# Kernel optimization log

Hardware: AMD Instinct MI355X
Metric: run time of the kernel (lower is better)

The kernel has to match this reference:

```python
import jax, jax.numpy as jnp
import numpy as np

PI = np.pi
NDIMS, K, M, F = 3, 513, 65536, 16
H = (K - 1) // 2  # 256; augmented factor has K = 2*H + 1 rows


def setup_inputs() -> dict:
    key = jax.random.key(0)
    k1, k2, k3, k4 = jax.random.split(key, 4)
    x = jax.random.uniform(k1, (M, NDIMS), dtype=jnp.float32)          # samples in [0,1]
    factors_real = jax.random.uniform(k2, (NDIMS, H, F), dtype=jnp.float32)
    factors_imag = 0.1 * jax.random.uniform(k3, (NDIMS, H, F), dtype=jnp.float32)
    lam = jnp.full((F,), 1.0 / F, dtype=jnp.float32)                   # f_vec init in torch
    return {"x": x, "factors_real": factors_real, "factors_imag": factors_imag, "lam": lam}


def _augment(fr, fi):
    # aug_fac real = [R; ones; flip(R)], imag = [I; zeros; -flip(I)]  -> (NDIMS, K, F)
    ones = jnp.ones((NDIMS, 1, F), fr.dtype)
    zeros = jnp.zeros((NDIMS, 1, F), fi.dtype)
    Ar = jnp.concatenate([fr, ones, jnp.flip(fr, axis=1)], axis=1)
    Ai = jnp.concatenate([fi, zeros, -jnp.flip(fi, axis=1)], axis=1)
    return Ar, Ai


def _conditionals(Ar, Ai):
    # c[n, f] = 1 / trapz(relu(Re(bb1^T aug_fac_n))[:, f], t),  t = linspace(0.01, 1, 100)
    T = 100
    t = jnp.linspace(0.01, 1.0, T, dtype=jnp.float32)
    kv = jnp.arange(-H, H + 1, dtype=jnp.float32)
    phi = (2.0 * PI) * kv[:, None] * t[None, :]                         # (K, T)
    # bb1 = exp(-i*phi): Re(bb1^T (Ar + i Ai)) = cos(phi)^T Ar + sin(phi)^T Ai
    y = (jnp.einsum('kt,nkf->ntf', jnp.cos(phi), Ar)
         + jnp.einsum('kt,nkf->ntf', jnp.sin(phi), Ai))
    y = jnp.maximum(y, 0.0)
    dt = jnp.float32((1.0 - 0.01) / (T - 1))
    integral = 0.5 * jnp.sum(y[:, 1:, :] + y[:, :-1, :], axis=1) * dt   # (NDIMS, F)
    return 1.0 / integral


def reference(x, factors_real, factors_imag, lam):
    Ar, Ai = _augment(factors_real, factors_imag)
    # torch computes c from detached data (numpy trapz) -> constant w.r.t. grads
    c = jax.lax.stop_gradient(_conditionals(Ar, Ai))                    # (NDIMS, F)
    kv = jnp.arange(-H, H + 1, dtype=jnp.float32)
    # basis = exp(-i*2pi*k*x): Re(basis^T A) = cos^T Ar + sin^T Ai
    theta = (2.0 * PI) * kv[None, :, None] * jnp.swapaxes(x, 0, 1)[:, None, :]  # (NDIMS, K, M)
    proj = (jnp.einsum('nkm,nkf->nmf', jnp.cos(theta), Ar)
            + jnp.einsum('nkm,nkf->nmf', jnp.sin(theta), Ai))           # (NDIMS, M, F)
    proj = jnp.maximum(proj, 0.0) * c[:, None, :]
    res = jnp.prod(proj, axis=0)                                        # (M, F)
    # sum(res @ diagflat(lam), dim=1) == res @ lam
    return res @ lam
```

## Files before the change

### kernel.cpp

```cpp
#include <hip/hip_runtime.h>

#define NDIMS 3
#define H_HALF 256
#define F_DIM 16
#define PI_F 3.14159265358979323846f

typedef _Float16 half8_t __attribute__((ext_vector_type(8)));
typedef __fp16 pk2_t __attribute__((ext_vector_type(2)));
typedef float float4_t __attribute__((ext_vector_type(4)));

#if __has_builtin(__builtin_amdgcn_fractf)
#define FRACT1(u) __builtin_amdgcn_fractf(u)
#else
#define FRACT1(u) ((u) - floorf(u))
#endif
#if __has_builtin(__builtin_amdgcn_sinf)
#define SIN2PI(u) __builtin_amdgcn_sinf(u)
#define COS2PI(u) __builtin_amdgcn_cosf(u)
#else
#define SIN2PI(u) __sinf(6.283185307f * (u))
#define COS2PI(u) __cosf(6.283185307f * (u))
#endif

static __device__ __forceinline__ unsigned int pk(float lo, float hi) {
    const pk2_t p = __builtin_amdgcn_cvt_pkrtz(lo, hi);
    return __builtin_bit_cast(unsigned int, p);
}

__global__ __launch_bounds__(256) void cond_partial_kernel(const float* __restrict__ fr,
                                                           const float* __restrict__ fi,
                                                           float* __restrict__ part_out) {
    const int n = blockIdx.x / 7;
    const int chunk = blockIdx.x % 7;
    const int tid = threadIdx.x;
    const int f = tid & 15;
    const int tq = tid >> 4;
    const int t_idx = chunk * 16 + tq;
    const float t = 0.01f + 0.01f * (float)t_idx;
    const float beta = 2.f * PI_F * t;
    const float cb = __cosf(beta), sb = __sinf(beta);
    float cj = cb, sj = sb;
    const float* frn = fr + n * H_HALF * F_DIM + f;
    const float* fin = fi + n * H_HALF * F_DIM + f;
    float acc = 0.f;
    #pragma unroll 8
    for (int j = 1; j <= H_HALF; ++j) {
        const int h = H_HALF - j;
        acc = fmaf(cj, frn[h * F_DIM], acc);
        acc = fmaf(-sj, fin[h * F_DIM], acc);
        const float cn = fmaf(cj, cb, -sj * sb);
        const float sn = fmaf(sj, cb, cj * sb);
        cj = cn; sj = sn;
    }
    const float y = fmaxf(fmaf(2.f, acc, 1.f), 0.f);
    const float wgt = (t_idx == 0 || t_idx == 99) ? 0.005f : 0.01f;
    float contrib = (t_idx < 100) ? wgt * y : 0.f;
    contrib += __shfl_xor(contrib, 16, 64);
    contrib += __shfl_xor(contrib, 32, 64);
    __shared__ float red[4][16];
    const int wv = tid >> 6;
    const int lane = tid & 63;
    if (lane < 16) red[wv][lane] = contrib;
    __syncthreads();
    if (tid < 16) {
        part_out[blockIdx.x * 16 + tid] =
            (red[0][tid] + red[1][tid]) + (red[2][tid] + red[3][tid]);
    }
}

__global__ __launch_bounds__(512, 4) void main_kernel(const float* __restrict__ x,
                                                      const float* __restrict__ fr,
                                                      const float* __restrict__ fi,
                                                      const float* __restrict__ lam,
                                                      const float* __restrict__ part,
                                                      float* __restrict__ out) {
    __shared__ __align__(16) unsigned int Bls[48 * 260];
    const int tid = threadIdx.x;

    #pragma unroll
    for (int r = 0; r < 24; ++r) {
        const int idx = r * 512 + tid;
        const int f = idx & 15;
        const int h = (idx >> 4) & 255;
        const int n = idx >> 12;
        Bls[(n * 16 + f) * 260 + (255 - h)] = pk(fr[idx], -fi[idx]);
    }
    __syncthreads();

    const int wave = tid >> 6;
    const int lane = tid & 63;
    const int l15 = lane & 15;
    const int q = lane >> 4;
    const int mbase = (blockIdx.x * 8 + wave) * 16;

    const float xv0 = x[(mbase + l15) * 3 + 0];
    const float xv1 = x[(mbase + l15) * 3 + 1];
    const float xv2 = x[(mbase + l15) * 3 + 2];

    float4_t accs[3];
    #pragma unroll
    for (int n = 0; n < 3; ++n) {
        const float xq = (n == 0) ? xv0 : (n == 1 ? xv1 : xv2);
        const float j0 = (float)(q * 4 + 1);
        const float u0 = FRACT1(j0 * xq);
        const float u1 = FRACT1((j0 + 1.f) * xq);
        const float u2 = FRACT1((j0 + 2.f) * xq);
        const float u3 = FRACT1((j0 + 3.f) * xq);
        float c0 = COS2PI(u0), s0 = SIN2PI(u0);
        float c1 = COS2PI(u1), s1 = SIN2PI(u1);
        float c2 = COS2PI(u2), s2 = SIN2PI(u2);
        float c3 = COS2PI(u3), s3 = SIN2PI(u3);
        const float ud = FRACT1(16.f * xq);
        const float cD = COS2PI(ud), sD = SIN2PI(ud);

        const unsigned int* Brow = &Bls[(n * 16 + l15) * 260 + q * 4];
        float4_t acc = {0.f, 0.f, 0.f, 0.f};
        #pragma unroll
        for (int s = 0; s < 16; ++s) {
            const int4 bv = *reinterpret_cast<const int4*>(Brow + s * 16);
            const half8_t bfrag = __builtin_bit_cast(half8_t, bv);
            const int4 av = { (int)pk(c0, s0), (int)pk(c1, s1),
                              (int)pk(c2, s2), (int)pk(c3, s3) };
            const half8_t afrag = __builtin_bit_cast(half8_t, av);
            acc = __builtin_amdgcn_mfma_f32_16x16x32_f16(afrag, bfrag, acc, 0, 0, 0);
            float t0 = fmaf(c0, cD, -s0 * sD); s0 = fmaf(s0, cD, c0 * sD); c0 = t0;
            float t1 = fmaf(c1, cD, -s1 * sD); s1 = fmaf(s1, cD, c1 * sD); c1 = t1;
            float t2 = fmaf(c2, cD, -s2 * sD); s2 = fmaf(s2, cD, c2 * sD); c2 = t2;
            float t3 = fmaf(c3, cD, -s3 * sD); s3 = fmaf(s3, cD, c3 * sD); c3 = t3;
        }
        accs[n] = acc;
    }

    const float lamv = lam[l15];
    float r0 = 1.f, r1 = 1.f, r2 = 1.f, r3 = 1.f;
    #pragma unroll
    for (int n = 0; n < 3; ++n) {
        float s = 0.f;
        #pragma unroll
        for (int c7 = 0; c7 < 7; ++c7) s += part[(n * 7 + c7) * 16 + l15];
        const float cc = 1.f / s;
        r0 *= fmaxf(fmaf(2.f, accs[n][0], 1.f), 0.f) * cc;
        r1 *= fmaxf(fmaf(2.f, accs[n][1], 1.f), 0.f) * cc;
        r2 *= fmaxf(fmaf(2.f, accs[n][2], 1.f), 0.f) * cc;
        r3 *= fmaxf(fmaf(2.f, accs[n][3], 1.f), 0.f) * cc;
    }
    r0 *= lamv; r1 *= lamv; r2 *= lamv; r3 *= lamv;
    #pragma unroll
    for (int off = 1; off < 16; off <<= 1) {
        r0 += __shfl_xor(r0, off, 64);
        r1 += __shfl_xor(r1, off, 64);
        r2 += __shfl_xor(r2, off, 64);
        r3 += __shfl_xor(r3, off, 64);
    }
    if (l15 == 0) {
        float4 o = { r0, r1, r2, r3 };
        *reinterpret_cast<float4*>(out + mbase + q * 4) = o;
    }
}

extern "C" void kernel_launch(void* const* d_in, const int* in_sizes, int n_in,
                              void* d_out, int out_size, void* d_ws, size_t ws_size,
                              hipStream_t stream) {
    const float* x   = (const float*)d_in[0];
    const float* fr  = (const float*)d_in[1];
    const float* fi  = (const float*)d_in[2];
    const float* lam = (const float*)d_in[3];
    float* out = (float*)d_out;
    float* part = (float*)d_ws;

    const int M = in_sizes[0] / NDIMS;

    cond_partial_kernel<<<NDIMS * 7, 256, 0, stream>>>(fr, fi, part);
    main_kernel<<<M / 128, 512, 0, stream>>>(x, fr, fi, lam, part, out);
}
```

Measured before the change: 80.60 us.

## Derive basis columns with packed fp16 rotations and vectorize factor staging loads

The inner MFMA loop now advances only one fp32 cos/sin pair per step. The other three columns are derived from it using packed half-precision FMAs with precomputed rotations by 1, 2 and 3 steps. This cuts the per-iteration fp32 rotation and pack work and aims to lower the VALU cost around each MFMA. It adds fp16 rounding error to the derived basis values. Two smaller changes come with it: the shared-memory staging of the factors uses float4 global loads, and the partial-integral and lam loads are hoisted ahead of the main loop so their latency overlaps compute.

```diff
diff --git a/kernel.cpp b/kernel.cpp
--- a/kernel.cpp
+++ b/kernel.cpp
@@ -6,6 +6,7 @@
 #define PI_F 3.14159265358979323846f
 
 typedef _Float16 half8_t __attribute__((ext_vector_type(8)));
+typedef _Float16 h2 __attribute__((ext_vector_type(2)));
 typedef __fp16 pk2_t __attribute__((ext_vector_type(2)));
 typedef float float4_t __attribute__((ext_vector_type(4)));
 
@@ -25,6 +26,10 @@
 static __device__ __forceinline__ unsigned int pk(float lo, float hi) {
     const pk2_t p = __builtin_amdgcn_cvt_pkrtz(lo, hi);
     return __builtin_bit_cast(unsigned int, p);
+}
+static __device__ __forceinline__ h2 pkh(float lo, float hi) {
+    const pk2_t p = __builtin_amdgcn_cvt_pkrtz(lo, hi);
+    return __builtin_bit_cast(h2, p);
 }
 
 __global__ __launch_bounds__(256) void cond_partial_kernel(const float* __restrict__ fr,
@@ -77,13 +82,23 @@
     __shared__ __align__(16) unsigned int Bls[48 * 260];
     const int tid = threadIdx.x;
 
-    #pragma unroll
-    for (int r = 0; r < 24; ++r) {
-        const int idx = r * 512 + tid;
-        const int f = idx & 15;
-        const int h = (idx >> 4) & 255;
-        const int n = idx >> 12;
-        Bls[(n * 16 + f) * 260 + (255 - h)] = pk(fr[idx], -fi[idx]);
+    {
+        const float4* fr4 = (const float4*)fr;
+        const float4* fi4 = (const float4*)fi;
+        #pragma unroll
+        for (int r = 0; r < 6; ++r) {
+            const int i4 = r * 512 + tid;
+            const float4 a = fr4[i4];
+            const float4 b = fi4[i4];
+            const int n = i4 >> 10;
+            const int h = (i4 >> 2) & 255;
+            const int f0 = (i4 & 3) * 4;
+            const int base = (n * 16 + f0) * 260 + (255 - h);
+            Bls[base      ] = pk(a.x, -b.x);
+            Bls[base + 260] = pk(a.y, -b.y);
+            Bls[base + 520] = pk(a.z, -b.z);
+            Bls[base + 780] = pk(a.w, -b.w);
+        }
     }
     __syncthreads();
 
@@ -96,22 +111,31 @@
     const float xv0 = x[(mbase + l15) * 3 + 0];
     const float xv1 = x[(mbase + l15) * 3 + 1];
     const float xv2 = x[(mbase + l15) * 3 + 2];
+    float psum[3];
+    #pragma unroll
+    for (int n = 0; n < 3; ++n) {
+        float s = 0.f;
+        #pragma unroll
+        for (int c7 = 0; c7 < 7; ++c7) s += part[(n * 7 + c7) * 16 + l15];
+        psum[n] = s;
+    }
+    const float lamv = lam[l15];
 
     float4_t accs[3];
     #pragma unroll
     for (int n = 0; n < 3; ++n) {
         const float xq = (n == 0) ? xv0 : (n == 1 ? xv1 : xv2);
-        const float j0 = (float)(q * 4 + 1);
-        const float u0 = FRACT1(j0 * xq);
-        const float u1 = FRACT1((j0 + 1.f) * xq);
-        const float u2 = FRACT1((j0 + 2.f) * xq);
-        const float u3 = FRACT1((j0 + 3.f) * xq);
-        float c0 = COS2PI(u0), s0 = SIN2PI(u0);
-        float c1 = COS2PI(u1), s1 = SIN2PI(u1);
-        float c2 = COS2PI(u2), s2 = SIN2PI(u2);
-        float c3 = COS2PI(u3), s3 = SIN2PI(u3);
+        const float u1 = FRACT1(xq);
+        const float cd1 = COS2PI(u1), sd1 = SIN2PI(u1);
+        const float cd2 = fmaf(cd1, cd1, -sd1 * sd1), sd2 = 2.f * sd1 * cd1;
+        const float cd3 = fmaf(cd2, cd1, -sd2 * sd1), sd3 = fmaf(sd2, cd1, cd2 * sd1);
+        const h2 cc1 = pkh(cd1, cd1), ns1 = pkh(-sd1, sd1);
+        const h2 cc2 = pkh(cd2, cd2), ns2 = pkh(-sd2, sd2);
+        const h2 cc3 = pkh(cd3, cd3), ns3 = pkh(-sd3, sd3);
         const float ud = FRACT1(16.f * xq);
         const float cD = COS2PI(ud), sD = SIN2PI(ud);
+        const float v0 = FRACT1((float)(q * 4 + 1) * xq);
+        float c0 = COS2PI(v0), s0 = SIN2PI(v0);
 
         const unsigned int* Brow = &Bls[(n * 16 + l15) * 260 + q * 4];
         float4_t acc = {0.f, 0.f, 0.f, 0.f};
@@ -119,26 +143,26 @@
         for (int s = 0; s < 16; ++s) {
             const int4 bv = *reinterpret_cast<const int4*>(Brow + s * 16);
             const half8_t bfrag = __builtin_bit_cast(half8_t, bv);
-            const int4 av = { (int)pk(c0, s0), (int)pk(c1, s1),
-                              (int)pk(c2, s2), (int)pk(c3, s3) };
+            const h2 b0 = pkh(c0, s0);
+            const h2 bsw = pkh(s0, c0);
+            const h2 d1 = __builtin_elementwise_fma(bsw, ns1, b0 * cc1);
+            const h2 d2 = __builtin_elementwise_fma(bsw, ns2, b0 * cc2);
+            const h2 d3 = __builtin_elementwise_fma(bsw, ns3, b0 * cc3);
+            const int4 av = { __builtin_bit_cast(int, b0), __builtin_bit_cast(int, d1),
+                              __builtin_bit_cast(int, d2), __builtin_bit_cast(int, d3) };
             const half8_t afrag = __builtin_bit_cast(half8_t, av);
             acc = __builtin_amdgcn_mfma_f32_16x16x32_f16(afrag, bfrag, acc, 0, 0, 0);
-            float t0 = fmaf(c0, cD, -s0 * sD); s0 = fmaf(s0, cD, c0 * sD); c0 = t0;
-            float t1 = fmaf(c1, cD, -s1 * sD); s1 = fmaf(s1, cD, c1 * sD); c1 = t1;
-            float t2 = fmaf(c2, cD, -s2 * sD); s2 = fmaf(s2, cD, c2 * sD); c2 = t2;
-            float t3 = fmaf(c3, cD, -s3 * sD); s3 = fmaf(s3, cD, c3 * sD); c3 = t3;
+            const float t0 = fmaf(c0, cD, -s0 * sD);
+            s0 = fmaf(s0, cD, c0 * sD);
+            c0 = t0;
         }
         accs[n] = acc;
     }
 
-    const float lamv = lam[l15];
     float r0 = 1.f, r1 = 1.f, r2 = 1.f, r3 = 1.f;
     #pragma unroll
     for (int n = 0; n < 3; ++n) {
-        float s = 0.f;
-        #pragma unroll
-        for (int c7 = 0; c7 < 7; ++c7) s += part[(n * 7 + c7) * 16 + l15];
-        const float cc = 1.f / s;
+        const float cc = 1.f / psum[n];
         r0 *= fmaxf(fmaf(2.f, accs[n][0], 1.f), 0.f) * cc;
         r1 *= fmaxf(fmaf(2.f, accs[n][1], 1.f), 0.f) * cc;
         r2 *= fmaxf(fmaf(2.f, accs[n][2], 1.f), 0.f) * cc;
```

Result: no change. 80.05 us (-0.7%).
